# Kernel optimization log

Hardware: AMD Instinct MI355X
Metric: run time of the kernel (lower is better)

The kernel has to match this reference:

```python
import jax, jax.numpy as jnp
import numpy as np

B, S, D, H = 4, 2048, 1024, 16
HD = D // H  # 64

def setup_inputs() -> dict:
    key = jax.random.key(0)
    ks = jax.random.split(key, 8)
    scale = 0.02
    return {
        "hidden_states": jax.random.normal(ks[0], (B, S, D), dtype=jnp.float32),
        "attention_mask": jnp.zeros((B, 1, 1, S), dtype=jnp.float32),
        "Wq": jax.random.normal(ks[1], (D, D), dtype=jnp.float32) * scale,
        "bq": jnp.zeros((D,), dtype=jnp.float32),
        "Wk": jax.random.normal(ks[2], (D, D), dtype=jnp.float32) * scale,
        "bk": jnp.zeros((D,), dtype=jnp.float32),
        "Wv": jax.random.normal(ks[3], (D, D), dtype=jnp.float32) * scale,
        "bv": jnp.zeros((D,), dtype=jnp.float32),
    }

def _split_heads(x):
    # [B,S,D] -> [B,H,S,HD]
    return x.reshape(B, S, H, HD).transpose(0, 2, 1, 3)

def reference(hidden_states, attention_mask, Wq, bq, Wk, bk, Wv, bv):
    q = _split_heads(hidden_states @ Wq.T + bq)
    k = _split_heads(hidden_states @ Wk.T + bk)
    v = _split_heads(hidden_states @ Wv.T + bv)
    scores = jnp.einsum('bhqd,bhkd->bhqk', q, k) / jnp.sqrt(jnp.float32(HD))
    scores = scores + attention_mask  # additive mask, broadcast [B,1,1,S]
    probs = jax.nn.softmax(scores, axis=-1)
    ctx = jnp.einsum('bhqk,bhkd->bhqd', probs, v)
    ctx = ctx.transpose(0, 2, 1, 3).reshape(B, S, D)
    return ctx
```

## Files before the change

### kernel.cpp

```cpp
#include <hip/hip_runtime.h>
#include <hip/hip_bf16.h>

typedef __bf16 bf16;
typedef __bf16 bf16x8 __attribute__((ext_vector_type(8)));
typedef __bf16 bf16x4 __attribute__((ext_vector_type(4)));
typedef float f32x4 __attribute__((ext_vector_type(4)));
typedef unsigned int u32;
typedef unsigned short u16;

constexpr int B_ = 4, S = 2048, D = 1024, H = 16, HD = 64;
constexpr int M = B_ * S;

#define MFMA(a, b, c) __builtin_amdgcn_mfma_f32_16x16x32_bf16(a, b, c, 0, 0, 0)

__device__ inline void gl_lds16(const bf16* g, bf16* l) {
  __builtin_amdgcn_global_load_lds(
      (const __attribute__((address_space(1))) u32*)g,
      (__attribute__((address_space(3))) u32*)l, 16, 0, 0);
}

__device__ inline bf16x8 load8(const void* base, size_t idx, bool isf32) {
  if (isf32) {
    const float* p = (const float*)base + idx;
    const float4 a = *(const float4*)p;
    const float4 b = *(const float4*)(p + 4);
    bf16x8 r;
    r[0] = (bf16)a.x; r[1] = (bf16)a.y; r[2] = (bf16)a.z; r[3] = (bf16)a.w;
    r[4] = (bf16)b.x; r[5] = (bf16)b.y; r[6] = (bf16)b.z; r[7] = (bf16)b.w;
    return r;
  }
  return *(const bf16x8*)((const bf16*)base + idx);
}
__device__ inline float load1(const void* base, size_t idx, bool isf32) {
  return isf32 ? ((const float*)base)[idx] : (float)((const bf16*)base)[idx];
}
__device__ inline f32x4 load4(const void* base, size_t idx, bool isf32) {
  if (isf32) {
    const float4 v = *(const float4*)((const float*)base + idx);
    return {v.x, v.y, v.z, v.w};
  }
  const bf16x4 v = *(const bf16x4*)((const bf16*)base + idx);
  return {(float)v[0], (float)v[1], (float)v[2], (float)v[3]};
}

__device__ inline int kvswz(int row) {
  return (((row & 3) | (((row >> 3) & 1) << 2)) << 4);
}
__device__ inline bf16x8 ldsf(const bf16* reg, int row, int cb) {
  return *(const bf16x8*)((const char*)reg + row * 128 + (cb ^ kvswz(row)));
}

__global__ __launch_bounds__(256) void detect_dtype(const uint4* __restrict__ X,
                                                    int* __restrict__ flag) {
  bool hit = false;
  for (int i = blockIdx.x * 256 + threadIdx.x; i < 32768; i += 64 * 256) {
    const uint4 v = X[i];
    const u32 w[4] = {v.x, v.y, v.z, v.w};
#pragma unroll
    for (int j = 0; j < 4; j++) {
      if (((w[j] >> 7) & 0xFFu) == 0xFFu) hit = true;
      if (((w[j] >> 23) & 0xFFu) == 0xFFu) hit = true;
    }
  }
  __shared__ int s;
  if (threadIdx.x == 0) s = 0;
  __syncthreads();
  if (hit) atomicOr(&s, 1);
  __syncthreads();
  if (threadIdx.x == 0 && s) atomicOr(flag, 1);
}

__global__ __launch_bounds__(256) void detect_mask(const uint4* __restrict__ Mk,
                                                   int* __restrict__ flag) {
  const bool isf32 = (*flag & 1) != 0;
  const int n4 = (B_ * S * (isf32 ? 4 : 2)) / 16;
  bool nz = false;
  for (int i = blockIdx.x * 256 + threadIdx.x; i < n4; i += 8 * 256) {
    const uint4 v = Mk[i];
    nz |= ((v.x | v.y | v.z | v.w) != 0u);
  }
  __shared__ int s;
  if (threadIdx.x == 0) s = 0;
  __syncthreads();
  if (nz) atomicOr(&s, 1);
  __syncthreads();
  if (threadIdx.x == 0 && s) atomicOr(flag, 2);
}

__global__ __launch_bounds__(256) void convert_inputs(
    const void* __restrict__ X, const void* __restrict__ W0,
    const void* __restrict__ W1, const void* __restrict__ W2,
    bf16* __restrict__ Xb, bf16* __restrict__ Wb,
    const int* __restrict__ flagp) {
  if ((*flagp & 1) == 0) return;
  const int seg = blockIdx.y;
  const size_t n = (seg == 0) ? (size_t)M * D : (size_t)D * D;
  const size_t i0 = ((size_t)blockIdx.x * 256 + threadIdx.x) * 8;
  if (i0 >= n) return;
  const void* src = seg == 0 ? X : seg == 1 ? W0 : seg == 2 ? W1 : W2;
  bf16* dst = seg == 0 ? Xb : Wb + (size_t)(seg - 1) * D * D;
  *(bf16x8*)(dst + i0) = load8(src, i0, true);
}

__global__ __launch_bounds__(256) void qkv_gemm(
    const void* __restrict__ X0, const bf16* __restrict__ Xb,
    const void* __restrict__ W0, const void* __restrict__ W1, const void* __restrict__ W2,
    const void* __restrict__ b0, const void* __restrict__ b1, const void* __restrict__ b2,
    bf16* __restrict__ Qo, bf16* __restrict__ Ko, bf16* __restrict__ Vo,
    const bf16* __restrict__ Wb, const int* __restrict__ flagp) {
  const int z = blockIdx.z;
  const bool isf32 = (*flagp & 1) != 0;
  const void* Worig = z == 0 ? W0 : z == 1 ? W1 : W2;
  const void* bias  = z == 0 ? b0 : z == 1 ? b1 : b2;
  bf16* out         = z == 0 ? Qo : z == 1 ? Ko : Vo;
  const bf16* Xs = isf32 ? Xb : (const bf16*)X0;
  const bf16* Ws = isf32 ? (Wb + (size_t)z * D * D) : (const bf16*)Worig;

  __shared__ __align__(16) bf16 As[128 * 32];
  __shared__ __align__(16) bf16 Bs[128 * 32];
  const int tid = threadIdx.x, lane = tid & 63, wave = tid >> 6;
  const int q16 = lane & 15, quad = lane >> 4;
  const int wm = (wave & 1) * 64, wn = (wave >> 1) * 64;
  const int bm = blockIdx.x * 128, bn = blockIdx.y * 128;
  const int r0 = tid >> 2, kg = (tid & 3) * 8;

  f32x4 acc[4][4] = {};

  for (int k0 = 0; k0 < D; k0 += 32) {
    __syncthreads();
    gl_lds16(Xs + (size_t)(bm + r0) * D + k0 + kg,      As + wave * 512 + lane * 8);
    gl_lds16(Xs + (size_t)(bm + 64 + r0) * D + k0 + kg, As + (4 + wave) * 512 + lane * 8);
    gl_lds16(Ws + (size_t)(bn + r0) * D + k0 + kg,      Bs + wave * 512 + lane * 8);
    gl_lds16(Ws + (size_t)(bn + 64 + r0) * D + k0 + kg, Bs + (4 + wave) * 512 + lane * 8);
    __syncthreads();
    bf16x8 af[4], bfr[4];
#pragma unroll
    for (int i = 0; i < 4; i++) {
      af[i]  = *(const bf16x8*)(As + (wm + i * 16 + q16) * 32 + quad * 8);
      bfr[i] = *(const bf16x8*)(Bs + (wn + i * 16 + q16) * 32 + quad * 8);
    }
#pragma unroll
    for (int mi = 0; mi < 4; mi++)
#pragma unroll
      for (int ni = 0; ni < 4; ni++)
        acc[mi][ni] = MFMA(af[mi], bfr[ni], acc[mi][ni]);
  }

  const float scl = (z == 0) ? 0.125f * 1.44269504f : 1.0f;
#pragma unroll
  for (int mi = 0; mi < 4; mi++) {
#pragma unroll
    for (int ni = 0; ni < 4; ni++) {
      const int gn = bn + wn + ni * 16 + q16;
      const float bb = load1(bias, gn, isf32);
      const int h = gn >> 6, hd = gn & 63;
      const int gm0 = bm + wm + mi * 16 + quad * 4;
      const int bidx = gm0 >> 11, s0 = gm0 & 2047;
      if (z == 2) {
        bf16x4 v4;
#pragma unroll
        for (int r = 0; r < 4; r++) v4[r] = (bf16)(acc[mi][ni][r] + bb);
        *(bf16x4*)(out + ((size_t)(bidx * H + h) * HD + hd) * S + s0) = v4;
      } else {
#pragma unroll
        for (int r = 0; r < 4; r++)
          out[((size_t)(bidx * H + h) * S + (s0 + r)) * HD + hd] = (bf16)((acc[mi][ni][r] + bb) * scl);
      }
    }
  }
}

__global__ __launch_bounds__(256, 4) void attn(
    const bf16* __restrict__ Q, const bf16* __restrict__ K,
    const bf16* __restrict__ Vt, const void* __restrict__ mask,
    void* __restrict__ outv, const int* __restrict__ flagp) {
  const int fl = *flagp;
  const bool isf32 = (fl & 1) != 0;
  const bool havemask = (fl & 2) != 0;
  const int tid = threadIdx.x, lane = tid & 63, wave = tid >> 6;
  const int q16 = lane & 15, quad = lane >> 4;

  const int bid = blockIdx.x;
  const int xcd = bid & 7, l = bid >> 3;
  const int bh = (xcd << 3) | (l & 7);
  const int qchunk = l >> 3;
  const int b = bh >> 4, h = bh & 15;
  const int qbase = qchunk * 128 + wave * 32;
  const float L2E = 1.44269504f;

  __shared__ __align__(16) bf16 kv[2][8192];

  bf16x8 qf[2][2];
#pragma unroll
  for (int qs = 0; qs < 2; qs++) {
    const bf16* qr = Q + ((size_t)bh * S + qbase + qs * 16 + q16) * HD;
    qf[qs][0] = *(const bf16x8*)(qr + quad * 8);
    qf[qs][1] = *(const bf16x8*)(qr + 32 + quad * 8);
  }

  f32x4 o[2][4] = {};
  float racc[2] = {};

  const bf16* Kb = K + (size_t)bh * S * HD;
  const bf16* Vb = Vt + (size_t)bh * HD * S;
  const int kprow = 8 * (q16 >> 2) + (q16 & 3);
  const size_t mbase = (size_t)b * S;

  const int srow8 = wave * 8 + (lane >> 3);
  const int pc = (lane & 7) * 16;
#define STAGE(BUFP_, T_)                                                       \
  {                                                                            \
    const int kt_ = (T_) * 64;                                                 \
    _Pragma("unroll") for (int i = 0; i < 2; i++) {                            \
      const int key = i * 32 + srow8;                                          \
      gl_lds16(Kb + (size_t)(kt_ + key) * HD + ((pc ^ kvswz(key)) >> 1),       \
               (BUFP_) + i * 2048 + wave * 512 + lane * 8);                    \
    }                                                                          \
    _Pragma("unroll") for (int i = 0; i < 2; i++) {                            \
      const int vrow = i * 32 + srow8;                                         \
      gl_lds16(Vb + (size_t)vrow * S + kt_ + ((pc ^ kvswz(vrow)) >> 1),        \
               (BUFP_) + 4096 + i * 2048 + wave * 512 + lane * 8);             \
    }                                                                          \
  }

  STAGE(&kv[0][0], 0);
  __syncthreads();

#pragma unroll 1
  for (int t = 0; t < 32; ++t) {
    if (t + 1 < 32) STAGE(&kv[(t + 1) & 1][0], t + 1);
    const bf16* Kl = &kv[t & 1][0];
    const bf16* Vl = Kl + 4096;
    const int kt = t * 64;

    bf16x8 kf[4][2];
#pragma unroll
    for (int ki = 0; ki < 4; ki++) {
      const int krow = 32 * (ki >> 1) + 4 * (ki & 1) + kprow;
      kf[ki][0] = ldsf(Kl, krow, quad * 16);
      kf[ki][1] = ldsf(Kl, krow, 64 + quad * 16);
    }

    bf16x8 pb[2][2];
#pragma unroll
    for (int qs = 0; qs < 2; qs++) {
      f32x4 sc[4];
      __builtin_amdgcn_s_setprio(1);
#pragma unroll
      for (int ki = 0; ki < 4; ki++) {
        f32x4 zz = {0.f, 0.f, 0.f, 0.f};
        zz = MFMA(kf[ki][0], qf[qs][0], zz);
        sc[ki] = MFMA(kf[ki][1], qf[qs][1], zz);
      }
      __builtin_amdgcn_s_setprio(0);
      float rs = 0.f;
#pragma unroll
      for (int ki = 0; ki < 4; ki++) {
        const int hh = ki >> 1, half = (ki & 1) * 4;
        float p0, p1, p2, p3;
        if (havemask) {
          f32x4 mv = load4(mask, mbase + kt + 32 * (ki >> 1) + 4 * (ki & 1) + 8 * quad, isf32);
          p0 = __builtin_amdgcn_exp2f(sc[ki][0] + mv[0] * L2E);
          p1 = __builtin_amdgcn_exp2f(sc[ki][1] + mv[1] * L2E);
          p2 = __builtin_amdgcn_exp2f(sc[ki][2] + mv[2] * L2E);
          p3 = __builtin_amdgcn_exp2f(sc[ki][3] + mv[3] * L2E);
        } else {
          p0 = __builtin_amdgcn_exp2f(sc[ki][0]);
          p1 = __builtin_amdgcn_exp2f(sc[ki][1]);
          p2 = __builtin_amdgcn_exp2f(sc[ki][2]);
          p3 = __builtin_amdgcn_exp2f(sc[ki][3]);
        }
        rs += ((p0 + p1) + (p2 + p3));
        pb[qs][hh][half + 0] = (bf16)p0; pb[qs][hh][half + 1] = (bf16)p1;
        pb[qs][hh][half + 2] = (bf16)p2; pb[qs][hh][half + 3] = (bf16)p3;
      }
      racc[qs] += rs;
    }

    __builtin_amdgcn_s_setprio(1);
#pragma unroll
    for (int hi = 0; hi < 4; hi++) {
      const int vrow = hi * 16 + q16;
      const bf16x8 v0 = ldsf(Vl, vrow, quad * 16);
      const bf16x8 v1 = ldsf(Vl, vrow, 64 + quad * 16);
      o[0][hi] = MFMA(v0, pb[0][0], o[0][hi]);
      o[0][hi] = MFMA(v1, pb[0][1], o[0][hi]);
      o[1][hi] = MFMA(v0, pb[1][0], o[1][hi]);
      o[1][hi] = MFMA(v1, pb[1][1], o[1][hi]);
    }
    __builtin_amdgcn_s_setprio(0);

    __syncthreads();
  }
#undef STAGE

#pragma unroll
  for (int qs = 0; qs < 2; qs++) {
    racc[qs] += __shfl_xor(racc[qs], 16);
    racc[qs] += __shfl_xor(racc[qs], 32);
  }

#pragma unroll
  for (int qs = 0; qs < 2; qs++) {
    const float inv = 1.0f / racc[qs];
    const size_t row = (size_t)b * S + qbase + qs * 16 + q16;
#pragma unroll
    for (int hi = 0; hi < 4; hi++) {
      const size_t off = row * D + h * HD + hi * 16 + quad * 4;
      if (isf32) {
        float4 st;
        st.x = o[qs][hi][0] * inv; st.y = o[qs][hi][1] * inv;
        st.z = o[qs][hi][2] * inv; st.w = o[qs][hi][3] * inv;
        *(float4*)((float*)outv + off) = st;
      } else {
        bf16x4 st;
#pragma unroll
        for (int r = 0; r < 4; r++) st[r] = (bf16)(o[qs][hi][r] * inv);
        *(bf16x4*)((bf16*)outv + off) = st;
      }
    }
  }
}

extern "C" void kernel_launch(void* const* d_in, const int* in_sizes, int n_in,
                              void* d_out, int out_size, void* d_ws, size_t ws_size,
                              hipStream_t stream) {
  const void* X    = d_in[0];
  const void* mask = d_in[1];
  const void* Wq = d_in[2]; const void* bq = d_in[3];
  const void* Wk = d_in[4]; const void* bk = d_in[5];
  const void* Wv = d_in[6]; const void* bv = d_in[7];

  const size_t elems = (size_t)M * D;
  bf16* Qw = (bf16*)d_ws;
  bf16* Kw = Qw + elems;
  bf16* Vw = Kw + elems;
  int* flag = (int*)(Vw + elems);

  bf16* Xb = (bf16*)d_out;
  bf16* Wb = Xb + elems;

  hipMemsetAsync(flag, 0, sizeof(int), stream);
  detect_dtype<<<64, 256, 0, stream>>>((const uint4*)X, flag);
  detect_mask<<<8, 256, 0, stream>>>((const uint4*)mask, flag);
  convert_inputs<<<dim3(4096, 4), 256, 0, stream>>>(X, Wq, Wk, Wv, Xb, Wb, flag);
  qkv_gemm<<<dim3(M / 128, D / 128, 3), 256, 0, stream>>>(
      X, Xb, Wq, Wk, Wv, bq, bk, bv, Qw, Kw, Vw, Wb, flag);
  attn<<<dim3(1024), 256, 0, stream>>>(Qw, Kw, Vw, mask, d_out, flag);
}
```

Baseline: 240.3 us.

## Double GEMM K-tile with XOR-swizzled LDS and compute softmax row sums via MFMA

The QKV GEMM now stages 64-wide K tiles instead of 32, which halves the number of barrier pairs per output tile. It also applies an XOR swizzle to the LDS layout so that fragment reads avoid bank conflicts. In the attention kernel, the per-lane VALU row-sum accumulation and the final cross-lane shuffles are replaced by extra MFMAs against a ones vector, moving that work from VALU to the matrix units. These are two unrelated changes; the trade-off is doubled LDS per GEMM block (occupancy risk) and four extra MFMAs per attention tile.

Result: slower. 246.1 us (+2.4%).

```diff
diff --git a/kernel.cpp b/kernel.cpp
--- a/kernel.cpp
+++ b/kernel.cpp
@@ -116,34 +116,44 @@
   const bf16* Xs = isf32 ? Xb : (const bf16*)X0;
   const bf16* Ws = isf32 ? (Wb + (size_t)z * D * D) : (const bf16*)Worig;
 
-  __shared__ __align__(16) bf16 As[128 * 32];
-  __shared__ __align__(16) bf16 Bs[128 * 32];
-  const int tid = threadIdx.x, lane = tid & 63, wave = tid >> 6;
+  __shared__ __align__(16) bf16 As[128 * 64];
+  __shared__ __align__(16) bf16 Bs[128 * 64];
+  const int tid = threadIdx.x, lane = tid & 63;
   const int q16 = lane & 15, quad = lane >> 4;
+  const int wave = tid >> 6;
   const int wm = (wave & 1) * 64, wn = (wave >> 1) * 64;
   const int bm = blockIdx.x * 128, bn = blockIdx.y * 128;
-  const int r0 = tid >> 2, kg = (tid & 3) * 8;
+
+  const int srow = tid >> 3;
+  const int scel = (((tid & 7) * 16) ^ ((srow & 7) << 4)) >> 1;
+  const int rswz = (q16 & 7) << 4;
 
   f32x4 acc[4][4] = {};
 
-  for (int k0 = 0; k0 < D; k0 += 32) {
+  for (int k0 = 0; k0 < D; k0 += 64) {
     __syncthreads();
-    gl_lds16(Xs + (size_t)(bm + r0) * D + k0 + kg,      As + wave * 512 + lane * 8);
-    gl_lds16(Xs + (size_t)(bm + 64 + r0) * D + k0 + kg, As + (4 + wave) * 512 + lane * 8);
-    gl_lds16(Ws + (size_t)(bn + r0) * D + k0 + kg,      Bs + wave * 512 + lane * 8);
-    gl_lds16(Ws + (size_t)(bn + 64 + r0) * D + k0 + kg, Bs + (4 + wave) * 512 + lane * 8);
+#pragma unroll
+    for (int j = 0; j < 4; j++)
+      gl_lds16(Xs + (size_t)(bm + j * 32 + srow) * D + k0 + scel, As + j * 2048 + tid * 8);
+#pragma unroll
+    for (int j = 0; j < 4; j++)
+      gl_lds16(Ws + (size_t)(bn + j * 32 + srow) * D + k0 + scel, Bs + j * 2048 + tid * 8);
     __syncthreads();
-    bf16x8 af[4], bfr[4];
-#pragma unroll
-    for (int i = 0; i < 4; i++) {
-      af[i]  = *(const bf16x8*)(As + (wm + i * 16 + q16) * 32 + quad * 8);
-      bfr[i] = *(const bf16x8*)(Bs + (wn + i * 16 + q16) * 32 + quad * 8);
-    }
-#pragma unroll
-    for (int mi = 0; mi < 4; mi++)
-#pragma unroll
-      for (int ni = 0; ni < 4; ni++)
-        acc[mi][ni] = MFMA(af[mi], bfr[ni], acc[mi][ni]);
+#pragma unroll
+    for (int kh = 0; kh < 2; kh++) {
+      bf16x8 af[4], bfr[4];
+#pragma unroll
+      for (int i = 0; i < 4; i++) {
+        const int cb = (kh * 64 + quad * 16) ^ rswz;
+        af[i]  = *(const bf16x8*)((const char*)As + (wm + i * 16 + q16) * 128 + cb);
+        bfr[i] = *(const bf16x8*)((const char*)Bs + (wn + i * 16 + q16) * 128 + cb);
+      }
+#pragma unroll
+      for (int mi = 0; mi < 4; mi++)
+#pragma unroll
+        for (int ni = 0; ni < 4; ni++)
+          acc[mi][ni] = MFMA(af[mi], bfr[ni], acc[mi][ni]);
+    }
   }
 
   const float scl = (z == 0) ? 0.125f * 1.44269504f : 1.0f;
@@ -198,8 +208,12 @@
     qf[qs][1] = *(const bf16x8*)(qr + 32 + quad * 8);
   }
 
+  bf16x8 ones;
+#pragma unroll
+  for (int j = 0; j < 8; j++) ones[j] = (bf16)1.0f;
+
   f32x4 o[2][4] = {};
-  float racc[2] = {};
+  f32x4 rsum[2] = {};
 
   const bf16* Kb = K + (size_t)bh * S * HD;
   const bf16* Vb = Vt + (size_t)bh * HD * S;
@@ -253,7 +267,6 @@
         sc[ki] = MFMA(kf[ki][1], qf[qs][1], zz);
       }
       __builtin_amdgcn_s_setprio(0);
-      float rs = 0.f;
 #pragma unroll
       for (int ki = 0; ki < 4; ki++) {
         const int hh = ki >> 1, half = (ki & 1) * 4;
@@ -270,11 +283,9 @@
           p2 = __builtin_amdgcn_exp2f(sc[ki][2]);
           p3 = __builtin_amdgcn_exp2f(sc[ki][3]);
         }
-        rs += ((p0 + p1) + (p2 + p3));
         pb[qs][hh][half + 0] = (bf16)p0; pb[qs][hh][half + 1] = (bf16)p1;
         pb[qs][hh][half + 2] = (bf16)p2; pb[qs][hh][half + 3] = (bf16)p3;
       }
-      racc[qs] += rs;
     }
 
     __builtin_amdgcn_s_setprio(1);
@@ -288,6 +299,10 @@
       o[1][hi] = MFMA(v0, pb[1][0], o[1][hi]);
       o[1][hi] = MFMA(v1, pb[1][1], o[1][hi]);
     }
+    rsum[0] = MFMA(ones, pb[0][0], rsum[0]);
+    rsum[0] = MFMA(ones, pb[0][1], rsum[0]);
+    rsum[1] = MFMA(ones, pb[1][0], rsum[1]);
+    rsum[1] = MFMA(ones, pb[1][1], rsum[1]);
     __builtin_amdgcn_s_setprio(0);
 
     __syncthreads();
@@ -296,13 +311,7 @@
 
 #pragma unroll
   for (int qs = 0; qs < 2; qs++) {
-    racc[qs] += __shfl_xor(racc[qs], 16);
-    racc[qs] += __shfl_xor(racc[qs], 32);
-  }
-
-#pragma unroll
-  for (int qs = 0; qs < 2; qs++) {
-    const float inv = 1.0f / racc[qs];
+    const float inv = 1.0f / rsum[qs][0];
     const size_t row = (size_t)b * S + qbase + qs * 16 + q16;
 #pragma unroll
     for (int hi = 0; hi < 4; hi++) {
```
